# Performance work log

Measured on AMD Instinct MI355X. Metric: run time of the kernel, lower is better.

## Reference

```python
import jax, jax.numpy as jnp
import numpy as np

B, N, F_IN, H, C = 4, 2048, 128, 4, 32
NEG_SLOPE = 0.2
EDGE_DENSITY = 0.01  # ~20 avg degree


def setup_inputs() -> dict:
    key = jax.random.key(0)
    ks = jax.random.split(key, 6)
    x = jax.random.normal(ks[0], (B, N, F_IN), dtype=jnp.float32)
    adj = (jax.random.uniform(ks[1], (B, N, N)) < EDGE_DENSITY).astype(jnp.float32)
    # glorot-style scaled params
    W = jax.random.normal(ks[2], (F_IN, H * C), dtype=jnp.float32) * (2.0 / (F_IN + H * C)) ** 0.5
    att_src = jax.random.normal(ks[3], (H, C), dtype=jnp.float32) * (2.0 / (1 + C)) ** 0.5
    att_dst = jax.random.normal(ks[4], (H, C), dtype=jnp.float32) * (2.0 / (1 + C)) ** 0.5
    bias = jnp.zeros((H * C,), dtype=jnp.float32)
    return {"x": x, "adj": adj, "W": W, "att_src": att_src, "att_dst": att_dst, "bias": bias}


def reference(x, adj, W, att_src, att_dst, bias):
    b, n, _ = x.shape
    h, c = att_src.shape
    # add self-loops
    idx = jnp.arange(n)
    adj = adj.at[:, idx, idx].set(1.0)
    # linear projection: [B,N,H,C]
    out = (x @ W).reshape(b, n, h, c)
    a_src = jnp.einsum('bnhc,hc->bnh', out, att_src)
    a_dst = jnp.einsum('bnhc,hc->bnh', out, att_dst)
    # alpha[b,i,j,h] = a_src[b,i,h] + a_dst[b,j,h]  -> [B,N,N,H]
    alpha = a_src[:, :, None, :] + a_dst[:, None, :, :]
    alpha = jax.nn.leaky_relu(alpha, NEG_SLOPE)
    alpha = adj[..., None] * jnp.exp(alpha)
    # faithful to original: normalize over dim=1 (the i axis)
    alpha = alpha / alpha.sum(axis=1, keepdims=True)
    # out_i = sum_j alpha[b,i,j,h] * feat[b,j,h,c]
    o = jnp.einsum('bijh,bjhc->bihc', alpha, out)
    o = o.reshape(b, n, h * c) + bias
    return o
```

## Files before the change

kernel.cpp:

```cpp
#include <hip/hip_runtime.h>
#include <math.h>

#define BB 4
#define NN 2048
#define F_IN 128
#define HH 4
#define CC 32
#define HC 128
#define NEG_SLOPE 0.2f
#define CAP 64
#define RT 64
#define CT 128
#define NRT 32
#define NCT 16
#define LCAP 320

__device__ __forceinline__ float lrelu(float v) {
    return v > 0.f ? v : NEG_SLOPE * v;
}

__global__ __launch_bounds__(256) void k_gemm_att(const float* __restrict__ x,
                                                  const float* __restrict__ W,
                                                  const float* __restrict__ att_src,
                                                  const float* __restrict__ att_dst,
                                                  float* __restrict__ feat,
                                                  float* __restrict__ a_src,
                                                  float* __restrict__ a_dst,
                                                  int* __restrict__ cnt) {
    __shared__ float xs[16][F_IN];
    __shared__ float fs[16][HC + 1];
    const long row0 = (long)blockIdx.x * 16;
    const int t = threadIdx.x;
    for (int idx = t; idx < 16 * F_IN; idx += 256)
        xs[idx >> 7][idx & 127] = x[row0 * F_IN + idx];
    __syncthreads();
    const int col = t & 127;
    const int rg  = t >> 7;
    float acc[8];
#pragma unroll
    for (int r = 0; r < 8; ++r) acc[r] = 0.f;
    for (int k = 0; k < F_IN; ++k) {
        float w = W[k * HC + col];
#pragma unroll
        for (int r = 0; r < 8; ++r)
            acc[r] += xs[rg + 2 * r][k] * w;
    }
#pragma unroll
    for (int r = 0; r < 8; ++r) {
        feat[(row0 + rg + 2 * r) * HC + col] = acc[r];
        fs[rg + 2 * r][col] = acc[r];
    }
    __syncthreads();
    if (t < 64) {
        const int row = t & 15;
        const int h   = t >> 4;
        float s = 0.f, d = 0.f;
#pragma unroll
        for (int c = 0; c < CC; ++c) {
            float v = fs[row][h * CC + c];
            s += v * att_src[h * CC + c];
            d += v * att_dst[h * CC + c];
        }
        a_src[(row0 + row) * 4 + h] = s;
        a_dst[(row0 + row) * 4 + h] = d;
    }
    if (t < 16) cnt[blockIdx.x * 16 + t] = 0;
}

__global__ __launch_bounds__(256) void k_tile(const float4* __restrict__ adj4,
                                              const float4* __restrict__ as4g,
                                              const float4* __restrict__ ad4g,
                                              int* __restrict__ cnt,
                                              unsigned short* __restrict__ nbr,
                                              float4* __restrict__ partial) {
    const int bx = blockIdx.x;
    const int b  = bx >> 9;
    const int rt = (bx >> 4) & 31;
    const int ct = bx & 15;
    const int i0 = rt * RT;
    const int c0 = ct * CT;
    const int t  = threadIdx.x;

    __shared__ float4 as4[RT];
    __shared__ float4 ad4[CT];
    __shared__ float4 pd[CT];
    __shared__ unsigned short blist[LCAP];
    __shared__ int rowcnt[RT];
    __shared__ int rowoff[RT];
    __shared__ int nent;

    const float4* p = adj4 + ((long)((b << 11) + i0) + (t >> 5)) * (NN / 4)
                    + (c0 >> 2) + (t & 31);
    float4 v[8];
#pragma unroll
    for (int s = 0; s < 8; ++s)
        v[s] = p[s * 8 * (NN / 4)];

    if (t < RT) {
        as4[t] = as4g[(b << 11) + i0 + t];
        rowcnt[t] = 0;
    }
    if (t < CT) {
        ad4[t] = ad4g[(b << 11) + c0 + t];
        pd[t] = make_float4(0.f, 0.f, 0.f, 0.f);
    }
    if (t == 0) nent = 0;
    __syncthreads();

    const int jb = (t & 31) * 4;
    const int rl = t >> 5;
#pragma unroll
    for (int s = 0; s < 8; ++s) {
        const int il = s * 8 + rl;
        const int gi = i0 + il;
#pragma unroll
        for (int k = 0; k < 4; ++k) {
            const float vv = (&v[s].x)[k];
            if (vv != 0.f || gi == c0 + jb + k) {
                int pos = atomicAdd(&nent, 1);
                if (pos < LCAP)
                    blist[pos] = (unsigned short)((il << 7) | (jb + k));
                atomicAdd(&rowcnt[il], 1);
            }
        }
    }
    __syncthreads();

    if (t < RT) {
        int rc = rowcnt[t];
        int bs = 0;
        if (rc > 0) bs = atomicAdd(&cnt[(b << 11) + i0 + t], rc);
        rowoff[t] = bs;
    }
    __syncthreads();

    const int ne = min(nent, LCAP);
    for (int e = t; e < ne; e += 256) {
        const int pk = blist[e];
        const int il = pk >> 7;
        const int jl = pk & 127;
        const float4 s4 = as4[il];
        const float4 d4 = ad4[jl];
        atomicAdd(&(&pd[jl].x)[0], __expf(lrelu(s4.x + d4.x)));
        atomicAdd(&(&pd[jl].x)[1], __expf(lrelu(s4.y + d4.y)));
        atomicAdd(&(&pd[jl].x)[2], __expf(lrelu(s4.z + d4.z)));
        atomicAdd(&(&pd[jl].x)[3], __expf(lrelu(s4.w + d4.w)));
        int slot = atomicAdd(&rowoff[il], 1);
        if (slot < CAP)
            nbr[((long)((b << 11) + i0 + il)) * CAP + slot] = (unsigned short)(c0 + jl);
    }
    __syncthreads();

    if (t < CT)
        partial[((long)(b * NRT + rt) << 11) + c0 + t] = pd[t];
}

__global__ __launch_bounds__(256) void k_rdenom(const float4* __restrict__ partial,
                                                float4* __restrict__ rdenom) {
    const int u = blockIdx.x * blockDim.x + threadIdx.x;
    if (u >= BB * NN) return;
    const int b = u >> 11;
    const int j = u & 2047;
    float4 s = make_float4(0.f, 0.f, 0.f, 0.f);
#pragma unroll
    for (int rt = 0; rt < NRT; ++rt) {
        float4 p = partial[((long)(b * NRT + rt) << 11) + j];
        s.x += p.x; s.y += p.y; s.z += p.z; s.w += p.w;
    }
    rdenom[u] = make_float4(1.f / s.x, 1.f / s.y, 1.f / s.z, 1.f / s.w);
}

__global__ __launch_bounds__(128) void k_aggr(const float* __restrict__ feat,
                                              const float* __restrict__ a_src,
                                              const float4* __restrict__ ad4,
                                              const float4* __restrict__ rd4,
                                              const int* __restrict__ cnt,
                                              const unsigned short* __restrict__ nbr,
                                              const float* __restrict__ bias,
                                              float* __restrict__ out) {
    const int bi = blockIdx.x;
    const int b  = bi >> 11;
    const int t  = threadIdx.x;
    __shared__ float4 s_coef[CAP];
    __shared__ int    s_j[CAP];
    __shared__ float  s_as[4];
    const int n = min(cnt[bi], CAP);
    if (t < 4) s_as[t] = a_src[bi * 4 + t];
    if (t < n) s_j[t] = nbr[(long)bi * CAP + t];
    __syncthreads();
    if (t < n) {
        const int j = s_j[t];
        const float4 ad = ad4[(b << 11) + j];
        const float4 rd = rd4[(b << 11) + j];
        float4 c;
        c.x = __expf(lrelu(s_as[0] + ad.x)) * rd.x;
        c.y = __expf(lrelu(s_as[1] + ad.y)) * rd.y;
        c.z = __expf(lrelu(s_as[2] + ad.z)) * rd.z;
        c.w = __expf(lrelu(s_as[3] + ad.w)) * rd.w;
        s_coef[t] = c;
    }
    __syncthreads();
    const int h = t >> 5;
    const float* fb = feat + ((long)(b << 11)) * HC + t;
    float a0 = 0.f, a1 = 0.f, a2 = 0.f, a3 = 0.f;
    float a4 = 0.f, a5 = 0.f, a6 = 0.f, a7 = 0.f;
    int s = 0;
    for (; s + 8 <= n; s += 8) {
        int j0 = s_j[s + 0], j1 = s_j[s + 1], j2 = s_j[s + 2], j3 = s_j[s + 3];
        int j4 = s_j[s + 4], j5 = s_j[s + 5], j6 = s_j[s + 6], j7 = s_j[s + 7];
        a0 += (&s_coef[s + 0].x)[h] * fb[(long)j0 * HC];
        a1 += (&s_coef[s + 1].x)[h] * fb[(long)j1 * HC];
        a2 += (&s_coef[s + 2].x)[h] * fb[(long)j2 * HC];
        a3 += (&s_coef[s + 3].x)[h] * fb[(long)j3 * HC];
        a4 += (&s_coef[s + 4].x)[h] * fb[(long)j4 * HC];
        a5 += (&s_coef[s + 5].x)[h] * fb[(long)j5 * HC];
        a6 += (&s_coef[s + 6].x)[h] * fb[(long)j6 * HC];
        a7 += (&s_coef[s + 7].x)[h] * fb[(long)j7 * HC];
    }
    for (; s < n; ++s)
        a0 += (&s_coef[s].x)[h] * fb[(long)s_j[s] * HC];
    out[(long)bi * HC + t] = ((a0 + a1) + (a2 + a3)) + ((a4 + a5) + (a6 + a7)) + bias[t];
}

extern "C" void kernel_launch(void* const* d_in, const int* in_sizes, int n_in,
                              void* d_out, int out_size, void* d_ws, size_t ws_size,
                              hipStream_t stream) {
    const float* x       = (const float*)d_in[0];
    const float* adj     = (const float*)d_in[1];
    const float* W       = (const float*)d_in[2];
    const float* att_src = (const float*)d_in[3];
    const float* att_dst = (const float*)d_in[4];
    const float* bias    = (const float*)d_in[5];
    float* out = (float*)d_out;

    float* feat    = (float*)d_ws;
    float* a_src   = feat    + (long)BB * NN * HC;
    float* a_dst   = a_src   + (long)BB * NN * HH;
    float* rdenom  = a_dst   + (long)BB * NN * HH;
    float* partial = rdenom  + (long)BB * NN * HH;
    int*   cnt     = (int*)(partial + (long)BB * NRT * NN * HH);
    unsigned short* nbr = (unsigned short*)(cnt + (long)BB * NN);

    k_gemm_att<<<(BB * NN) / 16, 256, 0, stream>>>(x, W, att_src, att_dst,
                                                   feat, a_src, a_dst, cnt);
    k_tile<<<BB * NRT * NCT, 256, 0, stream>>>((const float4*)adj, (const float4*)a_src,
                                               (const float4*)a_dst, cnt, nbr,
                                               (float4*)partial);
    k_rdenom<<<(BB * NN + 255) / 256, 256, 0, stream>>>((const float4*)partial,
                                                        (float4*)rdenom);
    k_aggr<<<BB * NN, 128, 0, stream>>>(feat, a_src, (const float4*)a_dst,
                                        (const float4*)rdenom, cnt, nbr, bias, out);
}
```

Measured before the change: 139.3 us.

## Replace global neighbor atomics with per-tile segmented neighbor lists and transpose GEMM tile

The tile kernel no longer builds a shared edge list and reserves slots with global atomics on per-row counters. Each column tile now writes up to 16 neighbors into its own fixed segment per row, plus a byte count per segment. The aggregation kernel compacts these segments with a prefix sum. The edge exponentials are computed directly in the scan loop, which removes an extra sync phase and the count-reset step. Separately, the GEMM stores x transposed in shared memory and reads it as float4. The risk is that neighbors are silently dropped if more than 16 fall into one row-tile segment, and the neighbor buffer becomes larger.

```diff
diff --git a/kernel.cpp b/kernel.cpp
--- a/kernel.cpp
+++ b/kernel.cpp
@@ -13,7 +13,7 @@
 #define CT 128
 #define NRT 32
 #define NCT 16
-#define LCAP 320
+#define SEG 16
 
 __device__ __forceinline__ float lrelu(float v) {
     return v > 0.f ? v : NEG_SLOPE * v;
@@ -25,30 +25,33 @@
                                                   const float* __restrict__ att_dst,
                                                   float* __restrict__ feat,
                                                   float* __restrict__ a_src,
-                                                  float* __restrict__ a_dst,
-                                                  int* __restrict__ cnt) {
-    __shared__ float xs[16][F_IN];
+                                                  float* __restrict__ a_dst) {
+    __shared__ float xs[F_IN][20];
     __shared__ float fs[16][HC + 1];
     const long row0 = (long)blockIdx.x * 16;
     const int t = threadIdx.x;
-    for (int idx = t; idx < 16 * F_IN; idx += 256)
-        xs[idx >> 7][idx & 127] = x[row0 * F_IN + idx];
+    for (int idx = t; idx < 16 * F_IN; idx += 256) {
+        const int row = idx >> 7, k = idx & 127;
+        xs[k][row] = x[row0 * F_IN + idx];
+    }
     __syncthreads();
     const int col = t & 127;
-    const int rg  = t >> 7;
+    const int rg  = (t >> 7) * 8;
     float acc[8];
 #pragma unroll
     for (int r = 0; r < 8; ++r) acc[r] = 0.f;
+#pragma unroll 4
     for (int k = 0; k < F_IN; ++k) {
-        float w = W[k * HC + col];
-#pragma unroll
-        for (int r = 0; r < 8; ++r)
-            acc[r] += xs[rg + 2 * r][k] * w;
+        const float w = W[k * HC + col];
+        const float4 xa = *(const float4*)&xs[k][rg];
+        const float4 xb = *(const float4*)&xs[k][rg + 4];
+        acc[0] += xa.x * w; acc[1] += xa.y * w; acc[2] += xa.z * w; acc[3] += xa.w * w;
+        acc[4] += xb.x * w; acc[5] += xb.y * w; acc[6] += xb.z * w; acc[7] += xb.w * w;
     }
 #pragma unroll
     for (int r = 0; r < 8; ++r) {
-        feat[(row0 + rg + 2 * r) * HC + col] = acc[r];
-        fs[rg + 2 * r][col] = acc[r];
+        feat[(row0 + rg + r) * HC + col] = acc[r];
+        fs[rg + r][col] = acc[r];
     }
     __syncthreads();
     if (t < 64) {
@@ -57,20 +60,19 @@
         float s = 0.f, d = 0.f;
 #pragma unroll
         for (int c = 0; c < CC; ++c) {
-            float v = fs[row][h * CC + c];
+            const float v = fs[row][h * CC + c];
             s += v * att_src[h * CC + c];
             d += v * att_dst[h * CC + c];
         }
         a_src[(row0 + row) * 4 + h] = s;
         a_dst[(row0 + row) * 4 + h] = d;
     }
-    if (t < 16) cnt[blockIdx.x * 16 + t] = 0;
 }
 
 __global__ __launch_bounds__(256) void k_tile(const float4* __restrict__ adj4,
                                               const float4* __restrict__ as4g,
                                               const float4* __restrict__ ad4g,
-                                              int* __restrict__ cnt,
+                                              unsigned char* __restrict__ cnt_seg,
                                               unsigned short* __restrict__ nbr,
                                               float4* __restrict__ partial) {
     const int bx = blockIdx.x;
@@ -84,10 +86,7 @@
     __shared__ float4 as4[RT];
     __shared__ float4 ad4[CT];
     __shared__ float4 pd[CT];
-    __shared__ unsigned short blist[LCAP];
-    __shared__ int rowcnt[RT];
-    __shared__ int rowoff[RT];
-    __shared__ int nent;
+    __shared__ int scnt[RT];
 
     const float4* p = adj4 + ((long)((b << 11) + i0) + (t >> 5)) * (NN / 4)
                     + (c0 >> 2) + (t & 31);
@@ -98,13 +97,12 @@
 
     if (t < RT) {
         as4[t] = as4g[(b << 11) + i0 + t];
-        rowcnt[t] = 0;
+        scnt[t] = 0;
     }
     if (t < CT) {
         ad4[t] = ad4g[(b << 11) + c0 + t];
         pd[t] = make_float4(0.f, 0.f, 0.f, 0.f);
     }
-    if (t == 0) nent = 0;
     __syncthreads();
 
     const int jb = (t & 31) * 4;
@@ -117,40 +115,24 @@
         for (int k = 0; k < 4; ++k) {
             const float vv = (&v[s].x)[k];
             if (vv != 0.f || gi == c0 + jb + k) {
-                int pos = atomicAdd(&nent, 1);
-                if (pos < LCAP)
-                    blist[pos] = (unsigned short)((il << 7) | (jb + k));
-                atomicAdd(&rowcnt[il], 1);
+                const int jl = jb + k;
+                const int slot = atomicAdd(&scnt[il], 1);
+                const float4 s4 = as4[il];
+                const float4 d4 = ad4[jl];
+                atomicAdd(&pd[jl].x, __expf(lrelu(s4.x + d4.x)));
+                atomicAdd(&pd[jl].y, __expf(lrelu(s4.y + d4.y)));
+                atomicAdd(&pd[jl].z, __expf(lrelu(s4.z + d4.z)));
+                atomicAdd(&pd[jl].w, __expf(lrelu(s4.w + d4.w)));
+                if (slot < SEG)
+                    nbr[(((long)((b << 11) + gi)) << 8) + (ct << 4) + slot] =
+                        (unsigned short)(c0 + jl);
             }
         }
     }
     __syncthreads();
 
-    if (t < RT) {
-        int rc = rowcnt[t];
-        int bs = 0;
-        if (rc > 0) bs = atomicAdd(&cnt[(b << 11) + i0 + t], rc);
-        rowoff[t] = bs;
-    }
-    __syncthreads();
-
-    const int ne = min(nent, LCAP);
-    for (int e = t; e < ne; e += 256) {
-        const int pk = blist[e];
-        const int il = pk >> 7;
-        const int jl = pk & 127;
-        const float4 s4 = as4[il];
-        const float4 d4 = ad4[jl];
-        atomicAdd(&(&pd[jl].x)[0], __expf(lrelu(s4.x + d4.x)));
-        atomicAdd(&(&pd[jl].x)[1], __expf(lrelu(s4.y + d4.y)));
-        atomicAdd(&(&pd[jl].x)[2], __expf(lrelu(s4.z + d4.z)));
-        atomicAdd(&(&pd[jl].x)[3], __expf(lrelu(s4.w + d4.w)));
-        int slot = atomicAdd(&rowoff[il], 1);
-        if (slot < CAP)
-            nbr[((long)((b << 11) + i0 + il)) * CAP + slot] = (unsigned short)(c0 + jl);
-    }
-    __syncthreads();
-
+    if (t < RT)
+        cnt_seg[(((b << 11) + i0 + t) << 4) + ct] = (unsigned char)min(scnt[t], SEG);
     if (t < CT)
         partial[((long)(b * NRT + rt) << 11) + c0 + t] = pd[t];
 }
@@ -164,7 +146,7 @@
     float4 s = make_float4(0.f, 0.f, 0.f, 0.f);
 #pragma unroll
     for (int rt = 0; rt < NRT; ++rt) {
-        float4 p = partial[((long)(b * NRT + rt) << 11) + j];
+        const float4 p = partial[((long)(b * NRT + rt) << 11) + j];
         s.x += p.x; s.y += p.y; s.z += p.z; s.w += p.w;
     }
     rdenom[u] = make_float4(1.f / s.x, 1.f / s.y, 1.f / s.z, 1.f / s.w);
@@ -174,7 +156,7 @@
                                               const float* __restrict__ a_src,
                                               const float4* __restrict__ ad4,
                                               const float4* __restrict__ rd4,
-                                              const int* __restrict__ cnt,
+                                              const unsigned char* __restrict__ cnt_seg,
                                               const unsigned short* __restrict__ nbr,
                                               const float* __restrict__ bias,
                                               float* __restrict__ out) {
@@ -184,10 +166,28 @@
     __shared__ float4 s_coef[CAP];
     __shared__ int    s_j[CAP];
     __shared__ float  s_as[4];
-    const int n = min(cnt[bi], CAP);
-    if (t < 4) s_as[t] = a_src[bi * 4 + t];
-    if (t < n) s_j[t] = nbr[(long)bi * CAP + t];
-    __syncthreads();
+    __shared__ int    s_cnt[16];
+    __shared__ int    s_pfx[17];
+    if (t < 16) s_cnt[t] = cnt_seg[(bi << 4) + t];
+    if (t < 4)  s_as[t] = a_src[bi * 4 + t];
+    __syncthreads();
+    if (t == 0) {
+        int a = 0;
+#pragma unroll
+        for (int s = 0; s < 16; ++s) { s_pfx[s] = a; a += s_cnt[s]; }
+        s_pfx[16] = a;
+    }
+    __syncthreads();
+#pragma unroll
+    for (int u = t; u < 256; u += 128) {
+        const int seg = u >> 4, k = u & 15;
+        if (k < s_cnt[seg]) {
+            const int pos = s_pfx[seg] + k;
+            if (pos < CAP) s_j[pos] = nbr[((long)bi << 8) + u];
+        }
+    }
+    __syncthreads();
+    const int n = min(s_pfx[16], CAP);
     if (t < n) {
         const int j = s_j[t];
         const float4 ad = ad4[(b << 11) + j];
@@ -206,8 +206,8 @@
     float a4 = 0.f, a5 = 0.f, a6 = 0.f, a7 = 0.f;
     int s = 0;
     for (; s + 8 <= n; s += 8) {
-        int j0 = s_j[s + 0], j1 = s_j[s + 1], j2 = s_j[s + 2], j3 = s_j[s + 3];
-        int j4 = s_j[s + 4], j5 = s_j[s + 5], j6 = s_j[s + 6], j7 = s_j[s + 7];
+        const int j0 = s_j[s + 0], j1 = s_j[s + 1], j2 = s_j[s + 2], j3 = s_j[s + 3];
+        const int j4 = s_j[s + 4], j5 = s_j[s + 5], j6 = s_j[s + 6], j7 = s_j[s + 7];
         a0 += (&s_coef[s + 0].x)[h] * fb[(long)j0 * HC];
         a1 += (&s_coef[s + 1].x)[h] * fb[(long)j1 * HC];
         a2 += (&s_coef[s + 2].x)[h] * fb[(long)j2 * HC];
@@ -238,16 +238,16 @@
     float* a_dst   = a_src   + (long)BB * NN * HH;
     float* rdenom  = a_dst   + (long)BB * NN * HH;
     float* partial = rdenom  + (long)BB * NN * HH;
-    int*   cnt     = (int*)(partial + (long)BB * NRT * NN * HH);
-    unsigned short* nbr = (unsigned short*)(cnt + (long)BB * NN);
+    unsigned char*  cnt_seg = (unsigned char*)(partial + (long)BB * NRT * NN * HH);
+    unsigned short* nbr = (unsigned short*)(cnt_seg + (long)BB * NN * NCT);
 
     k_gemm_att<<<(BB * NN) / 16, 256, 0, stream>>>(x, W, att_src, att_dst,
-                                                   feat, a_src, a_dst, cnt);
+                                                   feat, a_src, a_dst);
     k_tile<<<BB * NRT * NCT, 256, 0, stream>>>((const float4*)adj, (const float4*)a_src,
-                                               (const float4*)a_dst, cnt, nbr,
+                                               (const float4*)a_dst, cnt_seg, nbr,
                                                (float4*)partial);
     k_rdenom<<<(BB * NN + 255) / 256, 256, 0, stream>>>((const float4*)partial,
                                                         (float4*)rdenom);
     k_aggr<<<BB * NN, 128, 0, stream>>>(feat, a_src, (const float4*)a_dst,
-                                        (const float4*)rdenom, cnt, nbr, bias, out);
-}
+                                        (const float4*)rdenom, cnt_seg, nbr, bias, out);
+}
```

Measured after the change: 144.5 us. 1.04x slower.

## Fuse denominator reduction into aggregation and transpose x tile in GEMM

Applied to the files above, without the earlier changes.

Removes the separate k_rdenom launch. The partial column sums are stored transposed as [b][j][rt], so each aggregation block can reduce the 32 partials for its own neighbours with warp shuffles and compute the reciprocals in shared memory. It also stores the x tile k-major in shared memory so the GEMM can read eight consecutive rows with two float4 loads. In exchange, the reduction is now repeated for every neighbour of every row (about 20x redundant partial reads), and the transposed writes from k_tile are strided.

```diff
diff --git a/kernel.cpp b/kernel.cpp
--- a/kernel.cpp
+++ b/kernel.cpp
@@ -27,28 +27,32 @@
                                                   float* __restrict__ a_src,
                                                   float* __restrict__ a_dst,
                                                   int* __restrict__ cnt) {
-    __shared__ float xs[16][F_IN];
+    __shared__ float xs[F_IN][20];
     __shared__ float fs[16][HC + 1];
     const long row0 = (long)blockIdx.x * 16;
     const int t = threadIdx.x;
-    for (int idx = t; idx < 16 * F_IN; idx += 256)
-        xs[idx >> 7][idx & 127] = x[row0 * F_IN + idx];
+    for (int idx = t; idx < 16 * F_IN; idx += 256) {
+        const int row = idx >> 7, k = idx & 127;
+        xs[k][row] = x[row0 * F_IN + idx];
+    }
     __syncthreads();
     const int col = t & 127;
-    const int rg  = t >> 7;
+    const int rg  = (t >> 7) * 8;
     float acc[8];
 #pragma unroll
     for (int r = 0; r < 8; ++r) acc[r] = 0.f;
+#pragma unroll 4
     for (int k = 0; k < F_IN; ++k) {
-        float w = W[k * HC + col];
-#pragma unroll
-        for (int r = 0; r < 8; ++r)
-            acc[r] += xs[rg + 2 * r][k] * w;
+        const float w = W[k * HC + col];
+        const float4 xa = *(const float4*)&xs[k][rg];
+        const float4 xb = *(const float4*)&xs[k][rg + 4];
+        acc[0] += xa.x * w; acc[1] += xa.y * w; acc[2] += xa.z * w; acc[3] += xa.w * w;
+        acc[4] += xb.x * w; acc[5] += xb.y * w; acc[6] += xb.z * w; acc[7] += xb.w * w;
     }
 #pragma unroll
     for (int r = 0; r < 8; ++r) {
-        feat[(row0 + rg + 2 * r) * HC + col] = acc[r];
-        fs[rg + 2 * r][col] = acc[r];
+        feat[(row0 + rg + r) * HC + col] = acc[r];
+        fs[rg + r][col] = acc[r];
     }
     __syncthreads();
     if (t < 64) {
@@ -57,7 +61,7 @@
         float s = 0.f, d = 0.f;
 #pragma unroll
         for (int c = 0; c < CC; ++c) {
-            float v = fs[row][h * CC + c];
+            const float v = fs[row][h * CC + c];
             s += v * att_src[h * CC + c];
             d += v * att_dst[h * CC + c];
         }
@@ -152,28 +156,13 @@
     __syncthreads();
 
     if (t < CT)
-        partial[((long)(b * NRT + rt) << 11) + c0 + t] = pd[t];
-}
-
-__global__ __launch_bounds__(256) void k_rdenom(const float4* __restrict__ partial,
-                                                float4* __restrict__ rdenom) {
-    const int u = blockIdx.x * blockDim.x + threadIdx.x;
-    if (u >= BB * NN) return;
-    const int b = u >> 11;
-    const int j = u & 2047;
-    float4 s = make_float4(0.f, 0.f, 0.f, 0.f);
-#pragma unroll
-    for (int rt = 0; rt < NRT; ++rt) {
-        float4 p = partial[((long)(b * NRT + rt) << 11) + j];
-        s.x += p.x; s.y += p.y; s.z += p.z; s.w += p.w;
-    }
-    rdenom[u] = make_float4(1.f / s.x, 1.f / s.y, 1.f / s.z, 1.f / s.w);
+        partial[((((long)(b << 11)) + c0 + t) << 5) + rt] = pd[t];
 }
 
 __global__ __launch_bounds__(128) void k_aggr(const float* __restrict__ feat,
                                               const float* __restrict__ a_src,
                                               const float4* __restrict__ ad4,
-                                              const float4* __restrict__ rd4,
+                                              const float4* __restrict__ partial,
                                               const int* __restrict__ cnt,
                                               const unsigned short* __restrict__ nbr,
                                               const float* __restrict__ bias,
@@ -182,16 +171,34 @@
     const int b  = bi >> 11;
     const int t  = threadIdx.x;
     __shared__ float4 s_coef[CAP];
+    __shared__ float4 s_rd[CAP];
     __shared__ int    s_j[CAP];
     __shared__ float  s_as[4];
     const int n = min(cnt[bi], CAP);
     if (t < 4) s_as[t] = a_src[bi * 4 + t];
     if (t < n) s_j[t] = nbr[(long)bi * CAP + t];
     __syncthreads();
+
+    const int g = t >> 5, r = t & 31;
+    for (int s = g; s < n; s += 4) {
+        const int j = s_j[s];
+        float4 p = partial[((((long)(b << 11)) + j) << 5) + r];
+#pragma unroll
+        for (int off = 16; off; off >>= 1) {
+            p.x += __shfl_down(p.x, off, 32);
+            p.y += __shfl_down(p.y, off, 32);
+            p.z += __shfl_down(p.z, off, 32);
+            p.w += __shfl_down(p.w, off, 32);
+        }
+        if (r == 0)
+            s_rd[s] = make_float4(1.f / p.x, 1.f / p.y, 1.f / p.z, 1.f / p.w);
+    }
+    __syncthreads();
+
     if (t < n) {
         const int j = s_j[t];
         const float4 ad = ad4[(b << 11) + j];
-        const float4 rd = rd4[(b << 11) + j];
+        const float4 rd = s_rd[t];
         float4 c;
         c.x = __expf(lrelu(s_as[0] + ad.x)) * rd.x;
         c.y = __expf(lrelu(s_as[1] + ad.y)) * rd.y;
@@ -200,14 +207,15 @@
         s_coef[t] = c;
     }
     __syncthreads();
+
     const int h = t >> 5;
     const float* fb = feat + ((long)(b << 11)) * HC + t;
     float a0 = 0.f, a1 = 0.f, a2 = 0.f, a3 = 0.f;
     float a4 = 0.f, a5 = 0.f, a6 = 0.f, a7 = 0.f;
     int s = 0;
     for (; s + 8 <= n; s += 8) {
-        int j0 = s_j[s + 0], j1 = s_j[s + 1], j2 = s_j[s + 2], j3 = s_j[s + 3];
-        int j4 = s_j[s + 4], j5 = s_j[s + 5], j6 = s_j[s + 6], j7 = s_j[s + 7];
+        const int j0 = s_j[s + 0], j1 = s_j[s + 1], j2 = s_j[s + 2], j3 = s_j[s + 3];
+        const int j4 = s_j[s + 4], j5 = s_j[s + 5], j6 = s_j[s + 6], j7 = s_j[s + 7];
         a0 += (&s_coef[s + 0].x)[h] * fb[(long)j0 * HC];
         a1 += (&s_coef[s + 1].x)[h] * fb[(long)j1 * HC];
         a2 += (&s_coef[s + 2].x)[h] * fb[(long)j2 * HC];
@@ -236,9 +244,8 @@
     float* feat    = (float*)d_ws;
     float* a_src   = feat    + (long)BB * NN * HC;
     float* a_dst   = a_src   + (long)BB * NN * HH;
-    float* rdenom  = a_dst   + (long)BB * NN * HH;
-    float* partial = rdenom  + (long)BB * NN * HH;
-    int*   cnt     = (int*)(partial + (long)BB * NRT * NN * HH);
+    float* partial = a_dst   + (long)BB * NN * HH;
+    int*   cnt     = (int*)(partial + (long)BB * NN * NRT * 4);
     unsigned short* nbr = (unsigned short*)(cnt + (long)BB * NN);
 
     k_gemm_att<<<(BB * NN) / 16, 256, 0, stream>>>(x, W, att_src, att_dst,
@@ -246,8 +253,6 @@
     k_tile<<<BB * NRT * NCT, 256, 0, stream>>>((const float4*)adj, (const float4*)a_src,
                                                (const float4*)a_dst, cnt, nbr,
                                                (float4*)partial);
-    k_rdenom<<<(BB * NN + 255) / 256, 256, 0, stream>>>((const float4*)partial,
-                                                        (float4*)rdenom);
     k_aggr<<<BB * NN, 128, 0, stream>>>(feat, a_src, (const float4*)a_dst,
-                                        (const float4*)rdenom, cnt, nbr, bias, out);
-}
+                                        (const float4*)partial, cnt, nbr, bias, out);
+}
```

Measured after the change: 153.3 us. 1.1x slower.
